# Optimization experiments

Hardware: AMD Instinct MI355X
Metric: run time of the kernel (lower is better)

The kernel has to match this reference:

```python
import jax, jax.numpy as jnp
import numpy as np

B, N, D = 16, 4096, 256
EPS = 1e-6


def setup_inputs() -> dict:
    key = jax.random.key(0)
    kq, kk, kv, kwq, kwk, kbq, kbk = jax.random.split(key, 7)
    s = 1.0 / np.sqrt(D)
    return {
        "Q": jax.random.normal(kq, (B, N, D), dtype=jnp.float32),
        "K": jax.random.normal(kk, (B, N, D), dtype=jnp.float32),
        "V": jax.random.normal(kv, (B, N, D), dtype=jnp.float32),
        "Wq": jax.random.normal(kwq, (D, D), dtype=jnp.float32) * s,
        "bq": jax.random.normal(kbq, (D,), dtype=jnp.float32) * 0.01,
        "Wk": jax.random.normal(kwk, (D, D), dtype=jnp.float32) * s,
        "bk": jax.random.normal(kbk, (D,), dtype=jnp.float32) * 0.01,
    }


def reference(Q, K, V, Wq, bq, Wk, bk):
    # phi feature maps: sigmoid(Linear(dim, dim)) as in Flow-Attention
    phi_q = jax.nn.sigmoid(jnp.einsum("bnd,de->bne", Q, Wq) + bq)  # [B,N,D]
    phi_k = jax.nn.sigmoid(jnp.einsum("bnd,de->bne", K, Wk) + bk)  # [B,N,D]
    # O: column-normalized phi_k (over sequence); I: row-normalized phi_q (over features)
    O = phi_k / (jnp.sum(phi_k, axis=1, keepdims=True) + EPS)  # [B,N,D]
    I = phi_q / (jnp.sum(phi_q, axis=2, keepdims=True) + EPS)  # [B,N,D]
    # competition over the sequence dim
    V_b = jax.nn.softmax(O * V, axis=1)  # [B,N,D]
    # linear attention: (phi_k^T @ V_b) is the small [B,D,D] state
    KV = jnp.einsum("bnd,bne->bde", phi_k, V_b)  # [B,D,D]
    A = jnp.einsum("bnd,bde->bne", I, KV)  # [B,N,D]
    # sigmoid allocation gate
    R = jax.nn.sigmoid(jnp.sum(phi_q, axis=2, keepdims=True)) * A
    return R
```

## Files before the change

kernel.cpp:

```cpp
#include <hip/hip_runtime.h>
#include <cstddef>

#define EPS_ 1e-6f

typedef unsigned short u16;
typedef __attribute__((ext_vector_type(8))) short short8;
typedef __attribute__((ext_vector_type(8))) unsigned short us8;
typedef __attribute__((ext_vector_type(4))) unsigned short us4;
typedef __attribute__((ext_vector_type(4))) float f32x4;

__device__ __forceinline__ float sigmoidf_(float x){ return 1.0f/(1.0f+__expf(-x)); }
__device__ __forceinline__ float sigmoidf_fast(float x){
  return __builtin_amdgcn_rcpf(1.0f+__expf(-x));
}
__device__ __forceinline__ u16 f2bf(float x){
  union { __bf16 b; u16 u; } c; c.b = (__bf16)x; return c.u;
}
__device__ __forceinline__ float bf2f(u16 u){
  union { unsigned i; float f; } c; c.i = ((unsigned)u) << 16; return c.f;
}
__device__ __forceinline__ us4 cvt4(float4 v){
  us4 h; h[0]=f2bf(v.x); h[1]=f2bf(v.y); h[2]=f2bf(v.z); h[3]=f2bf(v.w); return h;
}

__global__ __launch_bounds__(256) void prep_w(const float* __restrict__ Wq,
                                              const float* __restrict__ Wk,
                                              u16* __restrict__ WqT,
                                              u16* __restrict__ WkT){
  const int m  = blockIdx.x >> 4;
  const int eb = blockIdx.x & 15;
  const float* W = m ? Wk : Wq;
  u16* WTf = m ? WkT : WqT;
  const int t = threadIdx.x;
  #pragma unroll
  for (int rep = 0; rep < 2; rep++) {
    const int lin  = rep*256 + t;
    const int it   = lin >> 6;
    const int lane = lin & 63;
    const int q    = lane >> 4;
    const int i16  = lane & 15;
    us8 o;
    #pragma unroll
    for (int j = 0; j < 8; j++)
      o[j] = f2bf(W[(it*32 + q*8 + j)*256 + eb*16 + i16]);
    *(us8*)&WTf[(size_t)((eb*8 + it)*512 + lane*8)] = o;
  }
}

__global__ __launch_bounds__(256, 3) void phi_both(
    const float* __restrict__ Q, const float* __restrict__ K,
    const u16* __restrict__ WqT, const u16* __restrict__ WkT,
    const float* __restrict__ bq, const float* __restrict__ bk,
    u16* __restrict__ phi_q, u16* __restrict__ phi_kT,
    float* __restrict__ rowsum, float* __restrict__ colsum)
{
  __shared__ union {
    u16 A[64][264];
    u16 S[64][264];
    u16 T2[128][136];
  } sh;

  const int t = threadIdx.x;
  const int l = t & 63;
  const int wf = t >> 6;
  const int i16 = l & 15, q = l >> 4;
  const int row0 = blockIdx.x * 64;
  const bool trans = (blockIdx.z != 0);

  const float* X    = trans ? K   : Q;
  const u16*  WT    = trans ? WkT : WqT;
  const float* bias = trans ? bk  : bq;

  {
    const int r0 = t >> 4;
    const int c0 = t & 15;
    #pragma unroll
    for (int half = 0; half < 2; half++) {
      float4 v[8];
      #pragma unroll
      for (int p = 0; p < 8; p++) {
        const int row = r0 + 16*(half*2 + (p >> 2));
        const int k4  = c0 + 16*(p & 3);
        v[p] = *(const float4*)&X[(size_t)(row0 + row)*256 + k4*4];
      }
      #pragma unroll
      for (int p = 0; p < 8; p++) {
        const int row = r0 + 16*(half*2 + (p >> 2));
        const int k4  = c0 + 16*(p & 3);
        *(us4*)&sh.A[row][k4*4] = cvt4(v[p]);
      }
    }
  }
  __syncthreads();

  f32x4 acc[4][4];
  #pragma unroll
  for (int i=0;i<4;i++)
    #pragma unroll
    for (int j=0;j<4;j++) acc[i][j] = (f32x4){0.f,0.f,0.f,0.f};

  const u16* wbf = WT + (size_t)wf*16384 + (size_t)l*8;
  short8 Bfr[3][4];
  #pragma unroll
  for (int fi=0;fi<4;fi++) Bfr[0][fi] = *(const short8*)&wbf[fi*4096];
  #pragma unroll
  for (int fi=0;fi<4;fi++) Bfr[1][fi] = *(const short8*)&wbf[fi*4096 + 512];

  #pragma unroll
  for (int it = 0; it < 8; it++) {
    if (it < 6) {
      #pragma unroll
      for (int fi=0;fi<4;fi++)
        Bfr[(it+2)%3][fi] = *(const short8*)&wbf[fi*4096 + (it+2)*512];
    }
    short8 af[4];
    #pragma unroll
    for (int mi=0;mi<4;mi++)
      af[mi] = *(const short8*)&sh.A[mi*16 + i16][it*32 + q*8];
    #pragma unroll
    for (int mi=0;mi<4;mi++)
      #pragma unroll
      for (int fi=0;fi<4;fi++)
        acc[mi][fi] = __builtin_amdgcn_mfma_f32_16x16x32_bf16(af[mi], Bfr[it%3][fi], acc[mi][fi], 0,0,0);
  }

  float bv[4];
  #pragma unroll
  for (int fi=0;fi<4;fi++) bv[fi] = bias[wf*64 + fi*16 + i16];

  __syncthreads();

  if (!trans) {
    #pragma unroll
    for (int mi=0;mi<4;mi++) {
      float rsub[4] = {0.f,0.f,0.f,0.f};
      #pragma unroll
      for (int fi=0;fi<4;fi++) {
        #pragma unroll
        for (int r=0;r<4;r++) {
          float ph = sigmoidf_fast(acc[mi][fi][r] + bv[fi]);
          rsub[r] += ph;
          sh.S[mi*16 + q*4 + r][wf*64 + fi*16 + i16] = f2bf(ph);
        }
      }
      #pragma unroll
      for (int r=0;r<4;r++) {
        float s = rsub[r];
        s += __shfl_xor(s,1); s += __shfl_xor(s,2); s += __shfl_xor(s,4); s += __shfl_xor(s,8);
        if (i16 == 0) atomicAdd(&rowsum[row0 + mi*16 + q*4 + r], s);
      }
    }
    __syncthreads();
    const size_t gbase = (size_t)row0 * 256;
    #pragma unroll
    for (int j=0;j<8;j++) {
      const int g = (j*256 + t) * 8;
      *(us8*)&phi_q[gbase + g] = *(const us8*)&sh.S[g >> 8][g & 255];
    }
  } else {
    const int b      = row0 >> 12;
    const int nchunk = (row0 & 4095) >> 6;
    #pragma unroll
    for (int h = 0; h < 2; h++) {
      if ((wf >> 1) == h) {
        #pragma unroll
        for (int fi=0;fi<4;fi++) {
          float cp = 0.f;
          #pragma unroll
          for (int mi=0;mi<4;mi++) {
            #pragma unroll
            for (int r=0;r<4;r++) {
              float ph = sigmoidf_fast(acc[mi][fi][r] + bv[fi]);
              cp += ph;
              sh.T2[(wf*64 + fi*16 + i16) & 127][mi*16 + q*4 + r] = f2bf(ph);
            }
          }
          cp += __shfl_xor(cp,16); cp += __shfl_xor(cp,32);
          if (l < 16) atomicAdd(&colsum[b*256 + wf*64 + fi*16 + l], cp);
        }
      }
      __syncthreads();
      const size_t gb = ((size_t)(b*64 + nchunk)*256 + h*128) * 64;
      #pragma unroll
      for (int j=0;j<4;j++) {
        const int g = (j*256 + t) * 8;
        *(us8*)&phi_kT[gb + g] = *(const us8*)&sh.T2[g >> 6][g & 63];
      }
      __syncthreads();
    }
  }
}

__global__ __launch_bounds__(256) void kv_kernel(const u16* __restrict__ phi_kT,
    const float* __restrict__ V, const float* __restrict__ colsum,
    u16* __restrict__ partsT, float* __restrict__ denom)
{
  __shared__ u16 phiT_lds[256][72];
  __shared__ u16 E_lds[64][72];

  const int t = threadIdx.x;
  const int l = t & 63;
  const int w = t >> 6;
  const int e0 = blockIdx.x * 64;
  const int nc = blockIdx.y;
  const int b  = blockIdx.z;
  const int i16 = l & 15, q = l >> 4;

  const int sd = t >> 3;
  const int sn = (t & 7) * 8;

  const size_t cbase = (size_t)(b*64 + nc*4) * 256 * 64;

  us8  rA[8];
  float rV[16];
  #pragma unroll
  for (int p=0;p<8;p++)
    rA[p] = *(const us8*)&phi_kT[cbase + (size_t)(sd + 32*p)*64 + sn];
  #pragma unroll
  for (int j=0;j<16;j++)
    rV[j] = V[(size_t)(b*4096 + nc*256 + w*16 + j)*256 + e0 + l];

  const float inv_cs = 1.0f / (colsum[b*256 + e0 + l] + EPS_);
  float dsum = 0.f;

  f32x4 acc[4][4];
  #pragma unroll
  for (int i=0;i<4;i++)
    #pragma unroll
    for (int j=0;j<4;j++) acc[i][j] = (f32x4){0.f,0.f,0.f,0.f};

  for (int c = 0; c < 4; c++) {
    #pragma unroll
    for (int p=0;p<8;p++) *(us8*)&phiT_lds[sd + 32*p][sn] = rA[p];
    __syncthreads();
    if (c < 3) {
      const size_t nb = cbase + (size_t)(c+1)*16384;
      #pragma unroll
      for (int p=0;p<8;p++)
        rA[p] = *(const us8*)&phi_kT[nb + (size_t)(sd + 32*p)*64 + sn];
    }
    us8 pv0 = *(const us8*)&phiT_lds[e0 + l][w*16];
    us8 pv1 = *(const us8*)&phiT_lds[e0 + l][w*16 + 8];
    us8 ev0, ev1;
    #pragma unroll
    for (int j=0;j<8;j++) {
      float ef = __expf(bf2f(pv0[j]) * inv_cs * rV[j]);
      dsum += ef; ev0[j] = f2bf(ef);
    }
    #pragma unroll
    for (int j=0;j<8;j++) {
      float ef = __expf(bf2f(pv1[j]) * inv_cs * rV[8+j]);
      dsum += ef; ev1[j] = f2bf(ef);
    }
    *(us8*)&E_lds[l][w*16]     = ev0;
    *(us8*)&E_lds[l][w*16 + 8] = ev1;
    if (c < 3) {
      #pragma unroll
      for (int j=0;j<16;j++)
        rV[j] = V[(size_t)(b*4096 + nc*256 + (c+1)*64 + w*16 + j)*256 + e0 + l];
    }
    __syncthreads();
    #pragma unroll
    for (int kk=0;kk<2;kk++){
      const int ko = kk*32 + q*8;
      short8 af[4], bfr[4];
      #pragma unroll
      for (int mi=0;mi<4;mi++) af[mi]  = *(const short8*)&phiT_lds[w*64 + mi*16 + i16][ko];
      #pragma unroll
      for (int ei=0;ei<4;ei++) bfr[ei] = *(const short8*)&E_lds[ei*16 + i16][ko];
      #pragma unroll
      for (int mi=0;mi<4;mi++)
        #pragma unroll
        for (int ei=0;ei<4;ei++)
          acc[mi][ei] = __builtin_amdgcn_mfma_f32_16x16x32_bf16(af[mi], bfr[ei], acc[mi][ei],0,0,0);
    }
    __syncthreads();
  }

  atomicAdd(&denom[b*256 + e0 + l], dsum);

  u16* slice = partsT + (size_t)(nc*16 + b) * 65536 + (size_t)blockIdx.x * 16384;
  #pragma unroll
  for (int mi=0;mi<4;mi++)
    #pragma unroll
    for (int ei=0;ei<4;ei++) {
      us4 o;
      #pragma unroll
      for (int r=0;r<4;r++) o[r] = f2bf(acc[mi][ei][r]);
      *(us4*)&slice[(size_t)(((w*16 + mi*4 + ei)*64 + l)*4)] = o;
    }
}

__global__ __launch_bounds__(256) void kv_norm(const u16* __restrict__ partsT,
    const float* __restrict__ denom, u16* __restrict__ KV_nT)
{
  const int t = threadIdx.x;
  const int b = blockIdx.y;
  const int s4 = blockIdx.x*256 + t;
  const int e0b = s4 >> 12;
  const int rem = s4 & 4095;
  const int comb = rem >> 6;
  const int l = rem & 63;
  const int w  = comb >> 4;
  const int mi = (comb >> 2) & 3;
  const int ei = comb & 3;
  const int e  = e0b*64 + ei*16 + (l & 15);
  const int d0 = w*64 + mi*16 + (l >> 4)*4;

  const float dn = denom[b*256 + e];
  float s0=0.f,s1=0.f,s2=0.f,s3=0.f;
  #pragma unroll 4
  for (int nc=0;nc<16;nc++){
    us4 v = *(const us4*)&partsT[(size_t)(nc*16 + b)*65536 + (size_t)s4*4];
    s0+=bf2f(v[0]); s1+=bf2f(v[1]); s2+=bf2f(v[2]); s3+=bf2f(v[3]);
  }
  us4 o; o[0]=f2bf(s0/dn); o[1]=f2bf(s1/dn); o[2]=f2bf(s2/dn); o[3]=f2bf(s3/dn);

  const int eb  = e >> 4;
  const int i16 = e & 15;
  const int it  = d0 >> 5;
  const int qo  = (d0 >> 3) & 3;
  const int j0  = d0 & 4;
  *(us4*)&KV_nT[(size_t)b*65536 + (size_t)((eb*8 + it)*512 + (qo*16 + i16)*8 + j0)] = o;
}

__global__ __launch_bounds__(256, 3) void out_gemm(const u16* __restrict__ phi_q,
    const u16* __restrict__ KV_nT, const float* __restrict__ rowsum,
    float* __restrict__ outp)
{
  __shared__ u16 A_lds[64][264];
  __shared__ float rs_lds[64];

  const int t = threadIdx.x;
  const int l = t & 63;
  const int we = t >> 6;
  const int i16 = l & 15, q = l >> 4;
  const int n0 = blockIdx.x * 64;
  const int b  = blockIdx.y;

  if (t < 64) rs_lds[t] = rowsum[b*4096 + n0 + t];

  {
    const size_t gbase = (size_t)(b*4096 + n0) * 256;
    us8 v[8];
    #pragma unroll
    for (int j=0;j<8;j++)
      v[j] = *(const us8*)&phi_q[gbase + (size_t)(j*256 + t)*8];
    #pragma unroll
    for (int j=0;j<8;j++) {
      const int g = (j*256 + t) * 8;
      *(us8*)&A_lds[g >> 8][g & 255] = v[j];
    }
  }
  __syncthreads();

  f32x4 acc[4][4];
  #pragma unroll
  for (int i=0;i<4;i++)
    #pragma unroll
    for (int j=0;j<4;j++) acc[i][j] = (f32x4){0.f,0.f,0.f,0.f};

  const u16* kbf = KV_nT + (size_t)b*65536 + (size_t)we*16384 + (size_t)l*8;
  short8 Bfr[3][4];
  #pragma unroll
  for (int ei=0;ei<4;ei++) Bfr[0][ei] = *(const short8*)&kbf[ei*4096];
  #pragma unroll
  for (int ei=0;ei<4;ei++) Bfr[1][ei] = *(const short8*)&kbf[ei*4096 + 512];

  #pragma unroll
  for (int it=0; it<8; it++){
    if (it < 6) {
      #pragma unroll
      for (int ei=0;ei<4;ei++)
        Bfr[(it+2)%3][ei] = *(const short8*)&kbf[ei*4096 + (it+2)*512];
    }
    short8 af[4];
    #pragma unroll
    for (int mi=0;mi<4;mi++)
      af[mi] = *(const short8*)&A_lds[mi*16 + i16][it*32 + q*8];
    #pragma unroll
    for (int mi=0;mi<4;mi++)
      #pragma unroll
      for (int ei=0;ei<4;ei++)
        acc[mi][ei] = __builtin_amdgcn_mfma_f32_16x16x32_bf16(af[mi], Bfr[it%3][ei], acc[mi][ei],0,0,0);
  }

  #pragma unroll
  for (int mi=0;mi<4;mi++){
    #pragma unroll
    for (int r=0;r<4;r++){
      const int nl = mi*16 + q*4 + r;
      const float rs = rs_lds[nl];
      const float gate = sigmoidf_(rs) / (rs + EPS_);
      #pragma unroll
      for (int ei=0;ei<4;ei++)
        outp[((size_t)(b*4096 + n0 + nl))*256 + we*64 + ei*16 + i16] = gate*acc[mi][ei][r];
    }
  }
}

extern "C" void kernel_launch(void* const* d_in, const int* in_sizes, int n_in,
                              void* d_out, int out_size, void* d_ws, size_t ws_size,
                              hipStream_t stream) {
  const float* Q  = (const float*)d_in[0];
  const float* K  = (const float*)d_in[1];
  const float* V  = (const float*)d_in[2];
  const float* Wq = (const float*)d_in[3];
  const float* bq = (const float*)d_in[4];
  const float* Wk = (const float*)d_in[5];
  const float* bk = (const float*)d_in[6];
  float* out = (float*)d_out;

  u16* phi_q  = (u16*)d_ws;
  u16* phi_kT = phi_q + 16777216;
  u16* WqT    = phi_kT + 16777216;
  u16* WkT    = WqT + 65536;
  float* colsum = (float*)(WkT + 65536);
  float* denom  = colsum + 4096;
  float* rowsum = denom + 4096;
  u16* partsT = (u16*)(rowsum + 65536);
  u16* KV_nT  = partsT + 16777216;

  hipMemsetAsync(colsum, 0, (4096 + 4096 + 65536) * sizeof(float), stream);

  prep_w<<<dim3(32), 256, 0, stream>>>(Wq, Wk, WqT, WkT);
  phi_both<<<dim3(1024, 1, 2), 256, 0, stream>>>(Q, K, WqT, WkT, bq, bk,
                                                 phi_q, phi_kT, rowsum, colsum);
  kv_kernel<<<dim3(4, 16, 16), 256, 0, stream>>>(phi_kT, V, colsum, partsT, denom);
  kv_norm<<<dim3(64, 16), 256, 0, stream>>>(partsT, denom, KV_nT);
  out_gemm<<<dim3(64, 16), 256, 0, stream>>>(phi_q, KV_nT, rowsum, out);
}
```

Before: 287.0 us.

## Fuse phi_q projection into output GEMM and drop phi_q round trip

```diff
diff --git a/kernel.cpp b/kernel.cpp
--- a/kernel.cpp
+++ b/kernel.cpp
@@ -47,16 +47,13 @@
   }
 }
 
-__global__ __launch_bounds__(256, 3) void phi_both(
-    const float* __restrict__ Q, const float* __restrict__ K,
-    const u16* __restrict__ WqT, const u16* __restrict__ WkT,
-    const float* __restrict__ bq, const float* __restrict__ bk,
-    u16* __restrict__ phi_q, u16* __restrict__ phi_kT,
-    float* __restrict__ rowsum, float* __restrict__ colsum)
+__global__ __launch_bounds__(256, 3) void phi_k(
+    const float* __restrict__ K, const u16* __restrict__ WkT,
+    const float* __restrict__ bk,
+    u16* __restrict__ phi_kT, float* __restrict__ colsum)
 {
   __shared__ union {
     u16 A[64][264];
-    u16 S[64][264];
     u16 T2[128][136];
   } sh;
 
@@ -65,11 +62,6 @@
   const int wf = t >> 6;
   const int i16 = l & 15, q = l >> 4;
   const int row0 = blockIdx.x * 64;
-  const bool trans = (blockIdx.z != 0);
-
-  const float* X    = trans ? K   : Q;
-  const u16*  WT    = trans ? WkT : WqT;
-  const float* bias = trans ? bk  : bq;
 
   {
     const int r0 = t >> 4;
@@ -81,7 +73,7 @@
       for (int p = 0; p < 8; p++) {
         const int row = r0 + 16*(half*2 + (p >> 2));
         const int k4  = c0 + 16*(p & 3);
-        v[p] = *(const float4*)&X[(size_t)(row0 + row)*256 + k4*4];
+        v[p] = *(const float4*)&K[(size_t)(row0 + row)*256 + k4*4];
       }
       #pragma unroll
       for (int p = 0; p < 8; p++) {
@@ -99,7 +91,7 @@
     #pragma unroll
     for (int j=0;j<4;j++) acc[i][j] = (f32x4){0.f,0.f,0.f,0.f};
 
-  const u16* wbf = WT + (size_t)wf*16384 + (size_t)l*8;
+  const u16* wbf = WkT + (size_t)wf*16384 + (size_t)l*8;
   short8 Bfr[3][4];
   #pragma unroll
   for (int fi=0;fi<4;fi++) Bfr[0][fi] = *(const short8*)&wbf[fi*4096];
@@ -126,68 +118,39 @@
 
   float bv[4];
   #pragma unroll
-  for (int fi=0;fi<4;fi++) bv[fi] = bias[wf*64 + fi*16 + i16];
+  for (int fi=0;fi<4;fi++) bv[fi] = bk[wf*64 + fi*16 + i16];
 
   __syncthreads();
 
-  if (!trans) {
-    #pragma unroll
-    for (int mi=0;mi<4;mi++) {
-      float rsub[4] = {0.f,0.f,0.f,0.f};
+  const int b      = row0 >> 12;
+  const int nchunk = (row0 & 4095) >> 6;
+  #pragma unroll
+  for (int h = 0; h < 2; h++) {
+    if ((wf >> 1) == h) {
       #pragma unroll
       for (int fi=0;fi<4;fi++) {
+        float cp = 0.f;
         #pragma unroll
-        for (int r=0;r<4;r++) {
-          float ph = sigmoidf_fast(acc[mi][fi][r] + bv[fi]);
-          rsub[r] += ph;
-          sh.S[mi*16 + q*4 + r][wf*64 + fi*16 + i16] = f2bf(ph);
+        for (int mi=0;mi<4;mi++) {
+          #pragma unroll
+          for (int r=0;r<4;r++) {
+            float ph = sigmoidf_fast(acc[mi][fi][r] + bv[fi]);
+            cp += ph;
+            sh.T2[(wf*64 + fi*16 + i16) & 127][mi*16 + q*4 + r] = f2bf(ph);
+          }
         }
-      }
-      #pragma unroll
-      for (int r=0;r<4;r++) {
-        float s = rsub[r];
-        s += __shfl_xor(s,1); s += __shfl_xor(s,2); s += __shfl_xor(s,4); s += __shfl_xor(s,8);
-        if (i16 == 0) atomicAdd(&rowsum[row0 + mi*16 + q*4 + r], s);
+        cp += __shfl_xor(cp,16); cp += __shfl_xor(cp,32);
+        if (l < 16) atomicAdd(&colsum[b*256 + wf*64 + fi*16 + l], cp);
       }
     }
     __syncthreads();
-    const size_t gbase = (size_t)row0 * 256;
-    #pragma unroll
-    for (int j=0;j<8;j++) {
+    const size_t gb = ((size_t)(b*64 + nchunk)*256 + h*128) * 64;
+    #pragma unroll
+    for (int j=0;j<4;j++) {
       const int g = (j*256 + t) * 8;
-      *(us8*)&phi_q[gbase + g] = *(const us8*)&sh.S[g >> 8][g & 255];
-    }
-  } else {
-    const int b      = row0 >> 12;
-    const int nchunk = (row0 & 4095) >> 6;
-    #pragma unroll
-    for (int h = 0; h < 2; h++) {
-      if ((wf >> 1) == h) {
-        #pragma unroll
-        for (int fi=0;fi<4;fi++) {
-          float cp = 0.f;
-          #pragma unroll
-          for (int mi=0;mi<4;mi++) {
-            #pragma unroll
-            for (int r=0;r<4;r++) {
-              float ph = sigmoidf_fast(acc[mi][fi][r] + bv[fi]);
-              cp += ph;
-              sh.T2[(wf*64 + fi*16 + i16) & 127][mi*16 + q*4 + r] = f2bf(ph);
-            }
-          }
-          cp += __shfl_xor(cp,16); cp += __shfl_xor(cp,32);
-          if (l < 16) atomicAdd(&colsum[b*256 + wf*64 + fi*16 + l], cp);
-        }
-      }
-      __syncthreads();
-      const size_t gb = ((size_t)(b*64 + nchunk)*256 + h*128) * 64;
-      #pragma unroll
-      for (int j=0;j<4;j++) {
-        const int g = (j*256 + t) * 8;
-        *(us8*)&phi_kT[gb + g] = *(const us8*)&sh.T2[g >> 6][g & 63];
-      }
-      __syncthreads();
-    }
+      *(us8*)&phi_kT[gb + g] = *(const us8*)&sh.T2[g >> 6][g & 63];
+    }
+    __syncthreads();
   }
 }
 
@@ -324,32 +287,45 @@
   *(us4*)&KV_nT[(size_t)b*65536 + (size_t)((eb*8 + it)*512 + (qo*16 + i16)*8 + j0)] = o;
 }
 
-__global__ __launch_bounds__(256, 3) void out_gemm(const u16* __restrict__ phi_q,
-    const u16* __restrict__ KV_nT, const float* __restrict__ rowsum,
+__global__ __launch_bounds__(256, 3) void out_fused(
+    const float* __restrict__ Q, const u16* __restrict__ WqT,
+    const float* __restrict__ bq, const u16* __restrict__ KV_nT,
     float* __restrict__ outp)
 {
-  __shared__ u16 A_lds[64][264];
-  __shared__ float rs_lds[64];
+  __shared__ union {
+    u16 A[64][264];
+    u16 S[64][264];
+  } sh;
+  __shared__ float rs_sh[64];
 
   const int t = threadIdx.x;
   const int l = t & 63;
-  const int we = t >> 6;
+  const int wf = t >> 6;
   const int i16 = l & 15, q = l >> 4;
   const int n0 = blockIdx.x * 64;
   const int b  = blockIdx.y;
 
-  if (t < 64) rs_lds[t] = rowsum[b*4096 + n0 + t];
+  if (t < 64) rs_sh[t] = 0.f;
 
   {
-    const size_t gbase = (size_t)(b*4096 + n0) * 256;
-    us8 v[8];
-    #pragma unroll
-    for (int j=0;j<8;j++)
-      v[j] = *(const us8*)&phi_q[gbase + (size_t)(j*256 + t)*8];
-    #pragma unroll
-    for (int j=0;j<8;j++) {
-      const int g = (j*256 + t) * 8;
-      *(us8*)&A_lds[g >> 8][g & 255] = v[j];
+    const int r0 = t >> 4;
+    const int c0 = t & 15;
+    const size_t gq = (size_t)(b*4096 + n0) * 256;
+    #pragma unroll
+    for (int half = 0; half < 2; half++) {
+      float4 v[8];
+      #pragma unroll
+      for (int p = 0; p < 8; p++) {
+        const int row = r0 + 16*(half*2 + (p >> 2));
+        const int k4  = c0 + 16*(p & 3);
+        v[p] = *(const float4*)&Q[gq + (size_t)row*256 + k4*4];
+      }
+      #pragma unroll
+      for (int p = 0; p < 8; p++) {
+        const int row = r0 + 16*(half*2 + (p >> 2));
+        const int k4  = c0 + 16*(p & 3);
+        *(us4*)&sh.A[row][k4*4] = cvt4(v[p]);
+      }
     }
   }
   __syncthreads();
@@ -360,29 +336,89 @@
     #pragma unroll
     for (int j=0;j<4;j++) acc[i][j] = (f32x4){0.f,0.f,0.f,0.f};
 
-  const u16* kbf = KV_nT + (size_t)b*65536 + (size_t)we*16384 + (size_t)l*8;
-  short8 Bfr[3][4];
-  #pragma unroll
-  for (int ei=0;ei<4;ei++) Bfr[0][ei] = *(const short8*)&kbf[ei*4096];
-  #pragma unroll
-  for (int ei=0;ei<4;ei++) Bfr[1][ei] = *(const short8*)&kbf[ei*4096 + 512];
+  {
+    const u16* wbf = WqT + (size_t)wf*16384 + (size_t)l*8;
+    short8 Bfr[3][4];
+    #pragma unroll
+    for (int fi=0;fi<4;fi++) Bfr[0][fi] = *(const short8*)&wbf[fi*4096];
+    #pragma unroll
+    for (int fi=0;fi<4;fi++) Bfr[1][fi] = *(const short8*)&wbf[fi*4096 + 512];
+
+    #pragma unroll
+    for (int it = 0; it < 8; it++) {
+      if (it < 6) {
+        #pragma unroll
+        for (int fi=0;fi<4;fi++)
+          Bfr[(it+2)%3][fi] = *(const short8*)&wbf[fi*4096 + (it+2)*512];
+      }
+      short8 af[4];
+      #pragma unroll
+      for (int mi=0;mi<4;mi++)
+        af[mi] = *(const short8*)&sh.A[mi*16 + i16][it*32 + q*8];
+      #pragma unroll
+      for (int mi=0;mi<4;mi++)
+        #pragma unroll
+        for (int fi=0;fi<4;fi++)
+          acc[mi][fi] = __builtin_amdgcn_mfma_f32_16x16x32_bf16(af[mi], Bfr[it%3][fi], acc[mi][fi], 0,0,0);
+    }
+  }
+
+  float bv[4];
+  #pragma unroll
+  for (int fi=0;fi<4;fi++) bv[fi] = bq[wf*64 + fi*16 + i16];
+
+  __syncthreads();
+
+  #pragma unroll
+  for (int mi=0;mi<4;mi++) {
+    float rsub[4] = {0.f,0.f,0.f,0.f};
+    #pragma unroll
+    for (int fi=0;fi<4;fi++) {
+      #pragma unroll
+      for (int r=0;r<4;r++) {
+        float ph = sigmoidf_fast(acc[mi][fi][r] + bv[fi]);
+        rsub[r] += ph;
+        sh.S[mi*16 + q*4 + r][wf*64 + fi*16 + i16] = f2bf(ph);
+      }
+    }
+    #pragma unroll
+    for (int r=0;r<4;r++) {
+      float s = rsub[r];
+      s += __shfl_xor(s,1); s += __shfl_xor(s,2); s += __shfl_xor(s,4); s += __shfl_xor(s,8);
+      if (i16 == 0) atomicAdd(&rs_sh[mi*16 + q*4 + r], s);
+    }
+  }
+
+  const u16* kbf = KV_nT + (size_t)b*65536 + (size_t)wf*16384 + (size_t)l*8;
+  short8 Bfr2[3][4];
+  #pragma unroll
+  for (int ei=0;ei<4;ei++) Bfr2[0][ei] = *(const short8*)&kbf[ei*4096];
+  #pragma unroll
+  for (int ei=0;ei<4;ei++) Bfr2[1][ei] = *(const short8*)&kbf[ei*4096 + 512];
+
+  __syncthreads();
+
+  #pragma unroll
+  for (int i=0;i<4;i++)
+    #pragma unroll
+    for (int j=0;j<4;j++) acc[i][j] = (f32x4){0.f,0.f,0.f,0.f};
 
   #pragma unroll
   for (int it=0; it<8; it++){
     if (it < 6) {
       #pragma unroll
       for (int ei=0;ei<4;ei++)
-        Bfr[(it+2)%3][ei] = *(const short8*)&kbf[ei*4096 + (it+2)*512];
+        Bfr2[(it+2)%3][ei] = *(const short8*)&kbf[ei*4096 + (it+2)*512];
     }
     short8 af[4];
     #pragma unroll
     for (int mi=0;mi<4;mi++)
-      af[mi] = *(const short8*)&A_lds[mi*16 + i16][it*32 + q*8];
+      af[mi] = *(const short8*)&sh.S[mi*16 + i16][it*32 + q*8];
     #pragma unroll
     for (int mi=0;mi<4;mi++)
       #pragma unroll
       for (int ei=0;ei<4;ei++)
-        acc[mi][ei] = __builtin_amdgcn_mfma_f32_16x16x32_bf16(af[mi], Bfr[it%3][ei], acc[mi][ei],0,0,0);
+        acc[mi][ei] = __builtin_amdgcn_mfma_f32_16x16x32_bf16(af[mi], Bfr2[it%3][ei], acc[mi][ei],0,0,0);
   }
 
   #pragma unroll
@@ -390,11 +426,11 @@
     #pragma unroll
     for (int r=0;r<4;r++){
       const int nl = mi*16 + q*4 + r;
-      const float rs = rs_lds[nl];
+      const float rs = rs_sh[nl];
       const float gate = sigmoidf_(rs) / (rs + EPS_);
       #pragma unroll
       for (int ei=0;ei<4;ei++)
-        outp[((size_t)(b*4096 + n0 + nl))*256 + we*64 + ei*16 + i16] = gate*acc[mi][ei][r];
+        outp[((size_t)(b*4096 + n0 + nl))*256 + wf*64 + ei*16 + i16] = gate*acc[mi][ei][r];
     }
   }
 }
@@ -411,22 +447,19 @@
   const float* bk = (const float*)d_in[6];
   float* out = (float*)d_out;
 
-  u16* phi_q  = (u16*)d_ws;
-  u16* phi_kT = phi_q + 16777216;
+  u16* phi_kT = (u16*)d_ws;
   u16* WqT    = phi_kT + 16777216;
   u16* WkT    = WqT + 65536;
   float* colsum = (float*)(WkT + 65536);
   float* denom  = colsum + 4096;
-  float* rowsum = denom + 4096;
-  u16* partsT = (u16*)(rowsum + 65536);
+  u16* partsT = (u16*)(denom + 4096);
   u16* KV_nT  = partsT + 16777216;
 
-  hipMemsetAsync(colsum, 0, (4096 + 4096 + 65536) * sizeof(float), stream);
+  hipMemsetAsync(colsum, 0, 8192 * sizeof(float), stream);
 
   prep_w<<<dim3(32), 256, 0, stream>>>(Wq, Wk, WqT, WkT);
-  phi_both<<<dim3(1024, 1, 2), 256, 0, stream>>>(Q, K, WqT, WkT, bq, bk,
-                                                 phi_q, phi_kT, rowsum, colsum);
+  phi_k<<<dim3(1024), 256, 0, stream>>>(K, WkT, bk, phi_kT, colsum);
   kv_kernel<<<dim3(4, 16, 16), 256, 0, stream>>>(phi_kT, V, colsum, partsT, denom);
   kv_norm<<<dim3(64, 16), 256, 0, stream>>>(partsT, denom, KV_nT);
-  out_gemm<<<dim3(64, 16), 256, 0, stream>>>(phi_q, KV_nT, rowsum, out);
-}
+  out_fused<<<dim3(64, 16), 256, 0, stream>>>(Q, WqT, bq, KV_nT, out);
+}
```

New measurement: 281.4 us. No clear change (-1.9%).
